# Optimization experiments

Measured on AMD Instinct MI355X. Metric: run time of the kernel, lower is better.

The kernel has to match this reference:

```python
import jax, jax.numpy as jnp
import numpy as np

N = 16384
E = 524288
H = 36
C = 16


def setup_inputs() -> dict:
    key = jax.random.key(0)
    ks = jax.random.split(key, 6)
    x = jax.random.normal(ks[0], (N, N), dtype=jnp.float32)
    edge_index = jax.random.randint(ks[1], (2, E), 0, N, dtype=jnp.int32)
    # Glorot-style init for the three GCN layer weights
    W1 = jax.random.normal(ks[2], (N, H), dtype=jnp.float32) * np.float32(np.sqrt(2.0 / (N + H)))
    W2 = jax.random.normal(ks[3], (H, H), dtype=jnp.float32) * np.float32(np.sqrt(2.0 / (H + H)))
    W3 = jax.random.normal(ks[4], (H, C), dtype=jnp.float32) * np.float32(np.sqrt(2.0 / (H + C)))
    b1 = jnp.zeros((H,), jnp.float32)
    b2 = jnp.zeros((H,), jnp.float32)
    b3 = jnp.zeros((C,), jnp.float32)
    return {"x": x, "edge_index": edge_index, "W1": W1, "b1": b1,
            "W2": W2, "b2": b2, "W3": W3, "b3": b3}


def _gcn_norm(edge_index, n):
    # PyG GCNConv: add self-loops, symmetric normalization D^-1/2 (A+I) D^-1/2
    loop = jnp.arange(n, dtype=edge_index.dtype)
    src = jnp.concatenate([edge_index[0], loop])  # message sources
    dst = jnp.concatenate([edge_index[1], loop])  # aggregation targets
    deg = jax.ops.segment_sum(jnp.ones(src.shape[0], jnp.float32), dst, num_segments=n)
    dis = jnp.where(deg > 0, jax.lax.rsqrt(jnp.maximum(deg, 1.0)), 0.0)
    norm = dis[src] * dis[dst]  # [E+N]
    return src, dst, norm


def reference(x, edge_index, W1, b1, W2, b2, W3, b3):
    n = x.shape[0]
    src, dst, norm = _gcn_norm(edge_index, n)

    def conv(h, W, b):
        h = h @ W                                   # linear transform first (thin GEMM)
        msg = h[src] * norm[:, None]                # gather + edge-wise scale
        agg = jax.ops.segment_sum(msg, dst, num_segments=n)  # scatter-add aggregate
        return agg + b

    h = jax.nn.relu(conv(x, W1, b1))
    # dropout is identity in eval mode
    h = jax.nn.relu(conv(h, W2, b2))
    h = conv(h, W3, b3)
    return jax.nn.softmax(h, axis=1)
```

## Files before the change

### kernel.cpp

```cpp
#include <hip/hip_runtime.h>

#define NN 16384
#define NE 524288
#define HID 36
#define NCLS 16
#define SPLITK 8
#define KSLICE (NN / SPLITK)

__global__ void k_zero_int(int* __restrict__ p, int n) {
  int i = blockIdx.x * blockDim.x + threadIdx.x;
  if (i < n) p[i] = 0;
}

__global__ void k_count(const int* __restrict__ dst, int* __restrict__ cnt) {
  int i = blockIdx.x * blockDim.x + threadIdx.x;
  if (i < NE) atomicAdd(&cnt[dst[i]], 1);
}

__global__ void k_scan(const int* __restrict__ cnt, int* __restrict__ off,
                       int* __restrict__ cur, float* __restrict__ dis) {
  __shared__ int part[256];
  const int t = threadIdx.x;
  const int base = t * 64;
  int s = 0;
  for (int i = 0; i < 64; ++i) s += cnt[base + i];
  part[t] = s;
  __syncthreads();
  if (t == 0) {
    int run = 0;
    for (int i = 0; i < 256; ++i) { int v = part[i]; part[i] = run; run += v; }
    off[NN] = run;
  }
  __syncthreads();
  int run = part[t];
  for (int i = 0; i < 64; ++i) {
    int idx = base + i;
    off[idx] = run;
    cur[idx] = run;
    run += cnt[idx];
    dis[idx] = rsqrtf((float)(cnt[idx] + 1));
  }
}

__global__ void k_scatter(const int* __restrict__ src, const int* __restrict__ dst,
                          int* __restrict__ cur, int* __restrict__ esrc) {
  int i = blockIdx.x * blockDim.x + threadIdx.x;
  if (i < NE) {
    int p = atomicAdd(&cur[dst[i]], 1);
    esrc[p] = src[i];
  }
}

__global__ void __launch_bounds__(256) k_gemm1(const float* __restrict__ x,
                                               const float* __restrict__ W,
                                               float* __restrict__ part) {
  const int rb = blockIdx.x & 63;
  const int s  = blockIdx.x >> 6;
  const int r  = rb * 256 + threadIdx.x;
  const int k0 = s * KSLICE;
  const float* __restrict__ a  = x + (size_t)r * NN + k0;
  const float* __restrict__ wp = W + (size_t)k0 * HID;
  float acc[HID];
#pragma unroll
  for (int c = 0; c < HID; ++c) acc[c] = 0.0f;
  for (int kk = 0; kk < KSLICE; kk += 16) {
    const float4 a0 = *(const float4*)(a + kk + 0);
    const float4 a1 = *(const float4*)(a + kk + 4);
    const float4 a2 = *(const float4*)(a + kk + 8);
    const float4 a3 = *(const float4*)(a + kk + 12);
    float av[16] = {a0.x, a0.y, a0.z, a0.w, a1.x, a1.y, a1.z, a1.w,
                    a2.x, a2.y, a2.z, a2.w, a3.x, a3.y, a3.z, a3.w};
    const float* __restrict__ wrow = wp + (size_t)kk * HID;
#pragma unroll
    for (int j = 0; j < 16; ++j) {
      const float aj = av[j];
#pragma unroll
      for (int c = 0; c < HID; ++c)
        acc[c] = fmaf(aj, wrow[j * HID + c], acc[c]);
    }
  }
  float* __restrict__ po = part + (size_t)s * NN * HID + (size_t)r * HID;
#pragma unroll
  for (int c4 = 0; c4 < HID / 4; ++c4)
    ((float4*)po)[c4] = make_float4(acc[4 * c4 + 0], acc[4 * c4 + 1],
                                    acc[4 * c4 + 2], acc[4 * c4 + 3]);
}

__global__ void k_reduce(const float* __restrict__ part, float* __restrict__ o, int n) {
  int i = blockIdx.x * blockDim.x + threadIdx.x;
  if (i < n) {
    float s = 0.0f;
#pragma unroll
    for (int p = 0; p < SPLITK; ++p) s += part[(size_t)p * n + i];
    o[i] = s;
  }
}

template <int F, bool RELU>
__global__ void k_agg(const float* __restrict__ h, const int* __restrict__ off,
                      const int* __restrict__ esrc, const float* __restrict__ dis,
                      const float* __restrict__ b, float* __restrict__ out) {
  const int tid = blockIdx.x * blockDim.x + threadIdx.x;
  const int i = tid / F;
  const int f = tid - i * F;
  const int beg = off[i], end = off[i + 1];
  float acc = 0.0f;
  for (int j = beg; j < end; ++j) {
    const int s = esrc[j];
    acc = fmaf(dis[s], h[(size_t)s * F + f], acc);
  }
  const float di = dis[i];
  float v = fmaf(di, acc, di * di * h[(size_t)i * F + f]) + b[f];
  if (RELU) v = fmaxf(v, 0.0f);
  out[tid] = v;
}

template <int IN, int OUT>
__global__ void k_mm(const float* __restrict__ h, const float* __restrict__ W,
                     float* __restrict__ o) {
  const int tid = blockIdx.x * blockDim.x + threadIdx.x;
  const int i = tid / OUT;
  const int c = tid - i * OUT;
  float acc = 0.0f;
#pragma unroll
  for (int k = 0; k < IN; ++k)
    acc = fmaf(h[(size_t)i * IN + k], W[k * OUT + c], acc);
  o[tid] = acc;
}

__global__ void k_softmax(const float* __restrict__ a, float* __restrict__ out) {
  const int i = blockIdx.x * blockDim.x + threadIdx.x;
  const float* __restrict__ p = a + (size_t)i * NCLS;
  float v[NCLS];
  float m = -3.0e38f;
#pragma unroll
  for (int c = 0; c < NCLS; ++c) { v[c] = p[c]; m = fmaxf(m, v[c]); }
  float s = 0.0f;
#pragma unroll
  for (int c = 0; c < NCLS; ++c) { v[c] = expf(v[c] - m); s += v[c]; }
  const float inv = 1.0f / s;
  float* __restrict__ q = out + (size_t)i * NCLS;
#pragma unroll
  for (int c = 0; c < NCLS; ++c) q[c] = v[c] * inv;
}

extern "C" void kernel_launch(void* const* d_in, const int* in_sizes, int n_in,
                              void* d_out, int out_size, void* d_ws, size_t ws_size,
                              hipStream_t stream) {
  const float* x  = (const float*)d_in[0];
  const int*   ei = (const int*)d_in[1];
  const float* W1 = (const float*)d_in[2];
  const float* b1 = (const float*)d_in[3];
  const float* W2 = (const float*)d_in[4];
  const float* b2 = (const float*)d_in[5];
  const float* W3 = (const float*)d_in[6];
  const float* b3 = (const float*)d_in[7];
  float* out = (float*)d_out;
  const int* e_src = ei;
  const int* e_dst = ei + NE;

  char* base = (char*)d_ws;
  size_t cur_off = 0;
  auto alloc = [&](size_t bytes) -> void* {
    void* p = base + cur_off;
    cur_off = (cur_off + bytes + 255) & ~(size_t)255;
    return p;
  };
  float* part = (float*)alloc((size_t)SPLITK * NN * HID * sizeof(float));
  float* h36  = (float*)alloc((size_t)NN * HID * sizeof(float));
  float* a36  = (float*)alloc((size_t)NN * HID * sizeof(float));
  float* h16  = (float*)alloc((size_t)NN * NCLS * sizeof(float));
  float* a16  = (float*)alloc((size_t)NN * NCLS * sizeof(float));
  int*   cnt  = (int*)alloc(NN * sizeof(int));
  int*   offs = (int*)alloc((NN + 1) * sizeof(int));
  int*   curp = (int*)alloc(NN * sizeof(int));
  int*   es   = (int*)alloc(NE * sizeof(int));
  float* dis  = (float*)alloc(NN * sizeof(float));

  k_zero_int<<<NN / 256, 256, 0, stream>>>(cnt, NN);
  k_count<<<NE / 256, 256, 0, stream>>>(e_dst, cnt);
  k_scan<<<1, 256, 0, stream>>>(cnt, offs, curp, dis);
  k_scatter<<<NE / 256, 256, 0, stream>>>(e_src, e_dst, curp, es);

  k_gemm1<<<SPLITK * (NN / 256), 256, 0, stream>>>(x, W1, part);
  k_reduce<<<NN * HID / 256, 256, 0, stream>>>(part, h36, NN * HID);
  k_agg<HID, true><<<NN * HID / 256, 256, 0, stream>>>(h36, offs, es, dis, b1, a36);

  k_mm<HID, HID><<<NN * HID / 256, 256, 0, stream>>>(a36, W2, h36);
  k_agg<HID, true><<<NN * HID / 256, 256, 0, stream>>>(h36, offs, es, dis, b2, a36);

  k_mm<HID, NCLS><<<NN * NCLS / 256, 256, 0, stream>>>(a36, W3, h16);
  k_agg<NCLS, false><<<NN * NCLS / 256, 256, 0, stream>>>(h16, offs, es, dis, b3, a16);
  k_softmax<<<NN / 256, 256, 0, stream>>>(a16, out);
}
```

Before: 1.966 ms.

## Stage x tiles through shared memory with coalesced loads and register prefetch

The first GEMM previously had each thread stream its own row of x with strided float4 loads, so a wavefront touched 64 different rows per access and coalescing was poor. Now a block loads a 256x32 tile cooperatively, eight threads per row-chunk, into padded LDS. The next chunk is prefetched into registers while the current one is computed. This adds two barriers per chunk and LDS reads in exchange for much better global memory access patterns on the 1 GB x read.

```diff
diff --git a/kernel.cpp b/kernel.cpp
--- a/kernel.cpp
+++ b/kernel.cpp
@@ -6,6 +6,8 @@
 #define NCLS 16
 #define SPLITK 8
 #define KSLICE (NN / SPLITK)
+#define RT 256
+#define KC 32
 
 __global__ void k_zero_int(int* __restrict__ p, int n) {
   int i = blockIdx.x * blockDim.x + threadIdx.x;
@@ -54,32 +56,60 @@
 __global__ void __launch_bounds__(256) k_gemm1(const float* __restrict__ x,
                                                const float* __restrict__ W,
                                                float* __restrict__ part) {
+  __shared__ float xs[RT][KC + 1];
   const int rb = blockIdx.x & 63;
   const int s  = blockIdx.x >> 6;
-  const int r  = rb * 256 + threadIdx.x;
+  const int t  = threadIdx.x;
+  const int r0 = rb * RT;
   const int k0 = s * KSLICE;
-  const float* __restrict__ a  = x + (size_t)r * NN + k0;
-  const float* __restrict__ wp = W + (size_t)k0 * HID;
+
+  const int srow = t >> 3;
+  const int sc4  = t & 7;
+  const float* __restrict__ xp =
+      x + (size_t)(r0 + srow) * NN + (size_t)k0 + (size_t)(sc4 * 4);
+
   float acc[HID];
 #pragma unroll
   for (int c = 0; c < HID; ++c) acc[c] = 0.0f;
-  for (int kk = 0; kk < KSLICE; kk += 16) {
-    const float4 a0 = *(const float4*)(a + kk + 0);
-    const float4 a1 = *(const float4*)(a + kk + 4);
-    const float4 a2 = *(const float4*)(a + kk + 8);
-    const float4 a3 = *(const float4*)(a + kk + 12);
-    float av[16] = {a0.x, a0.y, a0.z, a0.w, a1.x, a1.y, a1.z, a1.w,
-                    a2.x, a2.y, a2.z, a2.w, a3.x, a3.y, a3.z, a3.w};
-    const float* __restrict__ wrow = wp + (size_t)kk * HID;
-#pragma unroll
-    for (int j = 0; j < 16; ++j) {
-      const float aj = av[j];
+
+  float4 stg[8];
+#pragma unroll
+  for (int it = 0; it < 8; ++it)
+    stg[it] = *(const float4*)(xp + (size_t)(it * 32) * NN);
+#pragma unroll
+  for (int it = 0; it < 8; ++it) {
+    float* d = &xs[srow + it * 32][sc4 * 4];
+    d[0] = stg[it].x; d[1] = stg[it].y; d[2] = stg[it].z; d[3] = stg[it].w;
+  }
+  __syncthreads();
+
+  for (int kc = 0; kc < KSLICE; kc += KC) {
+    const int nxt = kc + KC;
+    if (nxt < KSLICE) {
+#pragma unroll
+      for (int it = 0; it < 8; ++it)
+        stg[it] = *(const float4*)(xp + nxt + (size_t)(it * 32) * NN);
+    }
+    const float* __restrict__ wk = W + (size_t)(k0 + kc) * HID;
+#pragma unroll
+    for (int kk = 0; kk < KC; ++kk) {
+      const float a = xs[t][kk];
 #pragma unroll
       for (int c = 0; c < HID; ++c)
-        acc[c] = fmaf(aj, wrow[j * HID + c], acc[c]);
+        acc[c] = fmaf(a, wk[kk * HID + c], acc[c]);
     }
-  }
-  float* __restrict__ po = part + (size_t)s * NN * HID + (size_t)r * HID;
+    if (nxt < KSLICE) {
+      __syncthreads();
+#pragma unroll
+      for (int it = 0; it < 8; ++it) {
+        float* d = &xs[srow + it * 32][sc4 * 4];
+        d[0] = stg[it].x; d[1] = stg[it].y; d[2] = stg[it].z; d[3] = stg[it].w;
+      }
+      __syncthreads();
+    }
+  }
+
+  float* __restrict__ po = part + (size_t)s * NN * HID + (size_t)(r0 + t) * HID;
 #pragma unroll
   for (int c4 = 0; c4 < HID / 4; ++c4)
     ((float4*)po)[c4] = make_float4(acc[4 * c4 + 0], acc[4 * c4 + 1],
@@ -182,7 +212,7 @@
   k_scan<<<1, 256, 0, stream>>>(cnt, offs, curp, dis);
   k_scatter<<<NE / 256, 256, 0, stream>>>(e_src, e_dst, curp, es);
 
-  k_gemm1<<<SPLITK * (NN / 256), 256, 0, stream>>>(x, W1, part);
+  k_gemm1<<<SPLITK * (NN / RT), 256, 0, stream>>>(x, W1, part);
   k_reduce<<<NN * HID / 256, 256, 0, stream>>>(part, h36, NN * HID);
   k_agg<HID, true><<<NN * HID / 256, 256, 0, stream>>>(h36, offs, es, dis, b1, a36);
 
```

Measured after the change: 2.195 ms. +11.6%, slower.
